# Performance work log

Measured on AMD Instinct MI355X. Metric: run time of the kernel, lower is better.

## Reference

```python
import jax, jax.numpy as jnp
import numpy as np

N, E, D = 100000, 600000, 128

def setup_inputs() -> dict:
    key = jax.random.key(0)
    ks = jax.random.split(key, 6)
    s = 1.0 / np.sqrt(D)
    return {
        "h": jax.random.normal(ks[0], (N, D), dtype=jnp.float32),
        "edge_index": jax.random.randint(ks[1], (2, E), 0, N, dtype=jnp.int64),
        "Wg": jax.random.normal(ks[2], (2 * D, D), dtype=jnp.float32) * s,
        "bg": jnp.zeros((D,), dtype=jnp.float32),
        "Ws": jax.random.normal(ks[3], (D, D), dtype=jnp.float32) * s,
        "bs": jnp.zeros((D,), dtype=jnp.float32),
        "Wr": jax.random.normal(ks[4], (D, D), dtype=jnp.float32) * s,
        "br": jnp.zeros((D,), dtype=jnp.float32),
    }

def reference(h, edge_index, Wg, bg, Ws, bs, Wr, br):
    send, rec = edge_index[0], edge_index[1]
    h_rec = h[rec]            # [E, D]
    h_send = h[send]          # [E, D]
    # gate: sigmoid(Linear(cat([h_rec, h_send])))  -- split W to avoid concat copy
    gate_in = h_rec @ Wg[:h.shape[1]] + h_send @ Wg[h.shape[1]:] + bg
    eta = jax.nn.sigmoid(gate_in)                      # [E, D]
    h_messages = eta * (h_send @ Ws + bs)              # [E, D]
    h_agg = jax.ops.segment_sum(h_messages, rec, num_segments=h.shape[0])
    return (h @ Wr + br) + h_agg
```

## Files before the change

### kernel.cpp

```cpp
#include <hip/hip_runtime.h>
#include <stdint.h>

#define FD 128

typedef __bf16 bf16x8 __attribute__((ext_vector_type(8)));
typedef unsigned short u16x8 __attribute__((ext_vector_type(8)));
typedef float  f32x16 __attribute__((ext_vector_type(16)));

__device__ __forceinline__ unsigned short f2bf(float f) {
    unsigned u = __float_as_uint(f);
    unsigned r = u + 0x7fffu + ((u >> 16) & 1u);
    return (unsigned short)(r >> 16);
}
__device__ __forceinline__ float bflo(unsigned u) { return __uint_as_float(u << 16); }
__device__ __forceinline__ float bfhi(unsigned u) { return __uint_as_float(u & 0xffff0000u); }


__global__ __launch_bounds__(256) void prep_kernel(
    const float* __restrict__ Wg,
    const float* __restrict__ Ws,
    const float* __restrict__ Wr,
    unsigned short* __restrict__ Wf)
{
    int wid = blockIdx.x * 256 + threadIdx.x;
    if (wid >= 512 * 128) return;
    int j  = wid & 7;
    int l  = (wid >> 3) & 63;
    int kt = (wid >> 9) & 7;
    int ct = wid >> 12;
    int k  = kt * 16 + (l >> 5) * 8 + j;
    int c  = ct * 32 + (l & 31);
    float v;
    if (c < 128)      v = Wg[k * FD + c];
    else if (c < 256) v = Wg[(128 + k) * FD + (c - 128)];
    else if (c < 384) v = Ws[k * FD + (c - 256)];
    else              v = Wr[k * FD + (c - 384)];
    Wf[wid] = f2bf(v);
}

__global__ __launch_bounds__(256, 4) void gemm_kernel(
    const float* __restrict__ h,
    const unsigned short* __restrict__ Wf,
    const float* __restrict__ bg,
    const float* __restrict__ bs,
    const float* __restrict__ br,
    unsigned short* __restrict__ A,
    unsigned short* __restrict__ BS,
    float* __restrict__ out,
    int N)
{
    __shared__ unsigned short Bsh[16384];

    const int w    = blockIdx.y;
    const int lane = threadIdx.x & 63;
    const int wid  = threadIdx.x >> 6;

    {
        const unsigned short* src = Wf + (size_t)w * 16384 + (size_t)threadIdx.x * 8;
        unsigned short* dst = Bsh + (size_t)threadIdx.x * 8;
        #pragma unroll
        for (int p = 0; p < 8; ++p) {
            __builtin_amdgcn_global_load_lds(
                (const __attribute__((address_space(1))) void*)(src + p * 2048),
                (__attribute__((address_space(3))) void*)(dst + p * 2048),
                16, 0, 0);
        }
    }

    const int col_l  = lane & 31;
    const int rhalf  = (lane >> 5) * 4;
    float bias[4];
    #pragma unroll
    for (int i = 0; i < 4; ++i) {
        int col = i * 32 + col_l;
        bias[i] = (w == 0) ? bg[col] : (w == 2) ? bs[col] : (w == 3) ? br[col] : 0.0f;
    }
    unsigned short* dst0 = (w == 0) ? A : (w == 2) ? (BS + 128) : BS;
    const size_t rstride = (w == 0) ? 128 : 256;

    __syncthreads();

    const int stride = gridDim.x * 128;
    for (int rb0 = blockIdx.x * 128; rb0 < N; rb0 += stride) {
        const int rb = rb0 + wid * 32;
        int arow = rb + (lane & 31);
        if (arow >= N) arow = N - 1;
        const float* aptr = h + (size_t)arow * FD + (lane >> 5) * 8;

        bf16x8 afrag[8];
        #pragma unroll
        for (int kt = 0; kt < 8; ++kt) {
            float4 f0 = *(const float4*)(aptr + kt * 16);
            float4 f1 = *(const float4*)(aptr + kt * 16 + 4);
            union { u16x8 u; bf16x8 b; } cv;
            cv.u[0] = f2bf(f0.x); cv.u[1] = f2bf(f0.y);
            cv.u[2] = f2bf(f0.z); cv.u[3] = f2bf(f0.w);
            cv.u[4] = f2bf(f1.x); cv.u[5] = f2bf(f1.y);
            cv.u[6] = f2bf(f1.z); cv.u[7] = f2bf(f1.w);
            afrag[kt] = cv.b;
        }

        f32x16 acc[4];
        #pragma unroll
        for (int i = 0; i < 4; ++i)
            #pragma unroll
            for (int r = 0; r < 16; ++r) acc[i][r] = 0.0f;

        #pragma unroll
        for (int kt = 0; kt < 8; ++kt) {
            #pragma unroll
            for (int i = 0; i < 4; ++i) {
                bf16x8 bfr = *(const bf16x8*)(Bsh + (size_t)((i * 8 + kt) * 64 + lane) * 8);
                acc[i] = __builtin_amdgcn_mfma_f32_32x32x16_bf16(
                             afrag[kt], bfr, acc[i], 0, 0, 0);
            }
        }

        const bool interior = (rb + 32 <= N);
        if (w == 3) {
            #pragma unroll
            for (int i = 0; i < 4; ++i) {
                int col = i * 32 + col_l;
                #pragma unroll
                for (int r = 0; r < 16; ++r) {
                    int row = rb + (r & 3) + 8 * (r >> 2) + rhalf;
                    if (interior || row < N)
                        out[(size_t)row * FD + col] = acc[i][r] + bias[i];
                }
            }
        } else {
            #pragma unroll
            for (int i = 0; i < 4; ++i) {
                int col = i * 32 + col_l;
                #pragma unroll
                for (int r = 0; r < 16; ++r) {
                    int row = rb + (r & 3) + 8 * (r >> 2) + rhalf;
                    if (interior || row < N)
                        dst0[(size_t)row * rstride + col] = f2bf(acc[i][r] + bias[i]);
                }
            }
        }
    }
}

__global__ __launch_bounds__(256) void hist_kernel(
    const int* __restrict__ idx, int* __restrict__ deg, int E)
{
    int e = blockIdx.x * 256 + threadIdx.x;
    if (e >= E) return;
    atomicAdd(&deg[idx[E + e]], 1);
}

__global__ __launch_bounds__(256) void scan1_kernel(
    const int* __restrict__ deg, int* __restrict__ partial, int N)
{
    __shared__ int sh[256];
    int base = blockIdx.x * 1024 + threadIdx.x * 4;
    int s = 0;
    #pragma unroll
    for (int j = 0; j < 4; ++j) s += (base + j < N) ? deg[base + j] : 0;
    sh[threadIdx.x] = s;
    __syncthreads();
    for (int ofs = 128; ofs > 0; ofs >>= 1) {
        if (threadIdx.x < ofs) sh[threadIdx.x] += sh[threadIdx.x + ofs];
        __syncthreads();
    }
    if (threadIdx.x == 0) partial[blockIdx.x] = sh[0];
}

__global__ __launch_bounds__(256) void scan2_kernel(int* __restrict__ partial, int nb)
{
    __shared__ int sh[256];
    int t = threadIdx.x;
    int p = (t < nb) ? partial[t] : 0;
    sh[t] = p;
    __syncthreads();
    for (int ofs = 1; ofs < 256; ofs <<= 1) {
        int x = (t >= ofs) ? sh[t - ofs] : 0;
        __syncthreads();
        sh[t] += x;
        __syncthreads();
    }
    if (t < nb) partial[t] = sh[t] - p;
}

__global__ __launch_bounds__(256) void scan3_kernel(
    int* __restrict__ deg, const int* __restrict__ partial, int N)
{
    __shared__ int sh[256];
    int base = blockIdx.x * 1024 + threadIdx.x * 4;
    int v[4];
    #pragma unroll
    for (int j = 0; j < 4; ++j) v[j] = (base + j < N) ? deg[base + j] : 0;
    int tsum = v[0] + v[1] + v[2] + v[3];
    sh[threadIdx.x] = tsum;
    __syncthreads();
    for (int ofs = 1; ofs < 256; ofs <<= 1) {
        int x = (threadIdx.x >= ofs) ? sh[threadIdx.x - ofs] : 0;
        __syncthreads();
        sh[threadIdx.x] += x;
        __syncthreads();
    }
    int run = partial[blockIdx.x] + sh[threadIdx.x] - tsum;
    #pragma unroll
    for (int j = 0; j < 4; ++j) {
        if (base + j < N) deg[base + j] = run;
        run += v[j];
    }
}

__global__ __launch_bounds__(256) void scatter_kernel(
    const int* __restrict__ idx, int* __restrict__ off,
    int* __restrict__ csr, int E)
{
    int e = blockIdx.x * 256 + threadIdx.x;
    if (e >= E) return;
    int s = idx[e];
    int r = idx[E + e];
    int pos = atomicAdd(&off[r], 1);
    csr[pos] = s;
}

__global__ __launch_bounds__(256) void aggregate_kernel(
    const int* __restrict__ off,
    const int* __restrict__ csr,
    const unsigned* __restrict__ A,
    const unsigned* __restrict__ BS,
    float* __restrict__ out,
    int N)
{
    int r = blockIdx.x * 4 + (threadIdx.x >> 6);
    if (r >= N) return;
    int lane = threadIdx.x & 63;

    int start = (r == 0) ? 0 : off[r - 1];
    int end   = off[r];
    if (start >= end) return;

    unsigned ua = A[(size_t)r * 64 + lane];
    float a0 = bflo(ua), a1 = bfhi(ua);
    float acc0 = 0.0f, acc1 = 0.0f;

    int i = start;
    for (; i + 3 < end; i += 4) {
        int s0 = csr[i], s1 = csr[i + 1], s2 = csr[i + 2], s3 = csr[i + 3];
        unsigned ub0 = BS[(size_t)s0 * 128 + lane];
        unsigned us0 = BS[(size_t)s0 * 128 + 64 + lane];
        unsigned ub1 = BS[(size_t)s1 * 128 + lane];
        unsigned us1 = BS[(size_t)s1 * 128 + 64 + lane];
        unsigned ub2 = BS[(size_t)s2 * 128 + lane];
        unsigned us2 = BS[(size_t)s2 * 128 + 64 + lane];
        unsigned ub3 = BS[(size_t)s3 * 128 + lane];
        unsigned us3 = BS[(size_t)s3 * 128 + 64 + lane];
        acc0 += bflo(us0) * __builtin_amdgcn_rcpf(1.0f + __expf(-(a0 + bflo(ub0))));
        acc1 += bfhi(us0) * __builtin_amdgcn_rcpf(1.0f + __expf(-(a1 + bfhi(ub0))));
        acc0 += bflo(us1) * __builtin_amdgcn_rcpf(1.0f + __expf(-(a0 + bflo(ub1))));
        acc1 += bfhi(us1) * __builtin_amdgcn_rcpf(1.0f + __expf(-(a1 + bfhi(ub1))));
        acc0 += bflo(us2) * __builtin_amdgcn_rcpf(1.0f + __expf(-(a0 + bflo(ub2))));
        acc1 += bfhi(us2) * __builtin_amdgcn_rcpf(1.0f + __expf(-(a1 + bfhi(ub2))));
        acc0 += bflo(us3) * __builtin_amdgcn_rcpf(1.0f + __expf(-(a0 + bflo(ub3))));
        acc1 += bfhi(us3) * __builtin_amdgcn_rcpf(1.0f + __expf(-(a1 + bfhi(ub3))));
    }
    for (; i < end; ++i) {
        int s0 = csr[i];
        unsigned ub0 = BS[(size_t)s0 * 128 + lane];
        unsigned us0 = BS[(size_t)s0 * 128 + 64 + lane];
        acc0 += bflo(us0) * __builtin_amdgcn_rcpf(1.0f + __expf(-(a0 + bflo(ub0))));
        acc1 += bfhi(us0) * __builtin_amdgcn_rcpf(1.0f + __expf(-(a1 + bfhi(ub0))));
    }

    float2* o = (float2*)(out + (size_t)r * FD + 2 * lane);
    float2 cur = *o;
    cur.x += acc0;
    cur.y += acc1;
    *o = cur;
}

extern "C" void kernel_launch(void* const* d_in, const int* in_sizes, int n_in,
                              void* d_out, int out_size, void* d_ws, size_t ws_size,
                              hipStream_t stream)
{
    const float* h  = (const float*)d_in[0];
    const int*   ei = (const int*)d_in[1];
    const float* Wg = (const float*)d_in[2];
    const float* bg = (const float*)d_in[3];
    const float* Ws = (const float*)d_in[4];
    const float* bs = (const float*)d_in[5];
    const float* Wr = (const float*)d_in[6];
    const float* br = (const float*)d_in[7];
    float* out = (float*)d_out;

    const int N = in_sizes[0] / FD;
    const int E = in_sizes[1] / 2;

    unsigned short* Wf  = (unsigned short*)d_ws;
    unsigned short* Abf = Wf + 512 * FD;
    unsigned short* BSb = Abf + (size_t)N * FD;
    int* deg     = (int*)(BSb + (size_t)N * 2 * FD);
    int* partial = deg + N;
    int* csr     = partial + 256;

    size_t need = (size_t)(512 * FD + 3ull * N * FD) * 2 + ((size_t)N + 256 + E) * 4;
    if (ws_size < need) return;

    const int nb = (N + 1023) / 1024;
    if (nb > 256) return;

    hipMemsetAsync(deg, 0, (size_t)N * 4, stream);

    prep_kernel<<<(512 * FD + 255) / 256, 256, 0, stream>>>(Wg, Ws, Wr, Wf);
    dim3 ggrid(256, 4);
    gemm_kernel<<<ggrid, 256, 0, stream>>>(h, Wf, bg, bs, br,
                                           Abf, BSb, out, N);
    hist_kernel<<<(E + 255) / 256, 256, 0, stream>>>(ei, deg, E);
    scan1_kernel<<<nb, 256, 0, stream>>>(deg, partial, N);
    scan2_kernel<<<1, 256, 0, stream>>>(partial, nb);
    scan3_kernel<<<nb, 256, 0, stream>>>(deg, partial, N);
    scatter_kernel<<<(E + 255) / 256, 256, 0, stream>>>(ei, deg, csr, E);
    aggregate_kernel<<<(N + 3) / 4, 256, 0, stream>>>(deg, csr,
                                                      (const unsigned*)Abf,
                                                      (const unsigned*)BSb,
                                                      out, N);
}
```

Measured before the change: 283.3 us.

## Fuse CSR build into one cooperative kernel with grid-wide syncs

Replaces the memset, histogram, three scan kernels and scatter with a single cooperative kernel of 1024 blocks that uses grid.sync between phases. This is meant to remove several kernel launch gaps and the separate memset. In exchange, each phase now runs grid-stride loops over fewer threads, and the grid barriers carry their own cost. The launch also depends on all 1024 blocks being co-resident.

```diff
diff --git a/kernel.cpp b/kernel.cpp
--- a/kernel.cpp
+++ b/kernel.cpp
@@ -1,5 +1,8 @@
 #include <hip/hip_runtime.h>
+#include <hip/hip_cooperative_groups.h>
 #include <stdint.h>
+
+namespace cg = cooperative_groups;
 
 #define FD 128
 
@@ -143,82 +146,85 @@
     }
 }
 
-__global__ __launch_bounds__(256) void hist_kernel(
-    const int* __restrict__ idx, int* __restrict__ deg, int E)
-{
-    int e = blockIdx.x * 256 + threadIdx.x;
-    if (e >= E) return;
-    atomicAdd(&deg[idx[E + e]], 1);
-}
-
-__global__ __launch_bounds__(256) void scan1_kernel(
-    const int* __restrict__ deg, int* __restrict__ partial, int N)
-{
+__global__ __launch_bounds__(256) void csr_kernel(
+    const int* __restrict__ idx,
+    int* __restrict__ deg,
+    int* __restrict__ partial,
+    int* __restrict__ csr,
+    int N, int E)
+{
+    cg::grid_group grid = cg::this_grid();
     __shared__ int sh[256];
-    int base = blockIdx.x * 1024 + threadIdx.x * 4;
-    int s = 0;
-    #pragma unroll
-    for (int j = 0; j < 4; ++j) s += (base + j < N) ? deg[base + j] : 0;
-    sh[threadIdx.x] = s;
-    __syncthreads();
-    for (int ofs = 128; ofs > 0; ofs >>= 1) {
-        if (threadIdx.x < ofs) sh[threadIdx.x] += sh[threadIdx.x + ofs];
+
+    const int tid  = blockIdx.x * 256 + threadIdx.x;
+    const int nthr = gridDim.x * 256;
+    const int nb   = (N + 1023) / 1024;
+
+    for (int i = tid; i < N; i += nthr) deg[i] = 0;
+    grid.sync();
+
+    for (int e = tid; e < E; e += nthr) atomicAdd(&deg[idx[E + e]], 1);
+    grid.sync();
+
+    if (blockIdx.x < nb) {
+        int base = blockIdx.x * 1024 + threadIdx.x * 4;
+        int s = 0;
+        #pragma unroll
+        for (int j = 0; j < 4; ++j) s += (base + j < N) ? deg[base + j] : 0;
+        sh[threadIdx.x] = s;
         __syncthreads();
-    }
-    if (threadIdx.x == 0) partial[blockIdx.x] = sh[0];
-}
-
-__global__ __launch_bounds__(256) void scan2_kernel(int* __restrict__ partial, int nb)
-{
-    __shared__ int sh[256];
-    int t = threadIdx.x;
-    int p = (t < nb) ? partial[t] : 0;
-    sh[t] = p;
-    __syncthreads();
-    for (int ofs = 1; ofs < 256; ofs <<= 1) {
-        int x = (t >= ofs) ? sh[t - ofs] : 0;
+        for (int ofs = 128; ofs > 0; ofs >>= 1) {
+            if (threadIdx.x < ofs) sh[threadIdx.x] += sh[threadIdx.x + ofs];
+            __syncthreads();
+        }
+        if (threadIdx.x == 0) partial[blockIdx.x] = sh[0];
+    }
+    grid.sync();
+
+    if (blockIdx.x == 0) {
+        int t = threadIdx.x;
+        int p = (t < nb) ? partial[t] : 0;
+        sh[t] = p;
         __syncthreads();
-        sh[t] += x;
+        for (int ofs = 1; ofs < 256; ofs <<= 1) {
+            int x = (t >= ofs) ? sh[t - ofs] : 0;
+            __syncthreads();
+            sh[t] += x;
+            __syncthreads();
+        }
+        if (t < nb) partial[t] = sh[t] - p;
+    }
+    grid.sync();
+
+    if (blockIdx.x < nb) {
+        int base = blockIdx.x * 1024 + threadIdx.x * 4;
+        int v[4];
+        #pragma unroll
+        for (int j = 0; j < 4; ++j) v[j] = (base + j < N) ? deg[base + j] : 0;
+        int tsum = v[0] + v[1] + v[2] + v[3];
+        sh[threadIdx.x] = tsum;
         __syncthreads();
-    }
-    if (t < nb) partial[t] = sh[t] - p;
-}
-
-__global__ __launch_bounds__(256) void scan3_kernel(
-    int* __restrict__ deg, const int* __restrict__ partial, int N)
-{
-    __shared__ int sh[256];
-    int base = blockIdx.x * 1024 + threadIdx.x * 4;
-    int v[4];
-    #pragma unroll
-    for (int j = 0; j < 4; ++j) v[j] = (base + j < N) ? deg[base + j] : 0;
-    int tsum = v[0] + v[1] + v[2] + v[3];
-    sh[threadIdx.x] = tsum;
-    __syncthreads();
-    for (int ofs = 1; ofs < 256; ofs <<= 1) {
-        int x = (threadIdx.x >= ofs) ? sh[threadIdx.x - ofs] : 0;
-        __syncthreads();
-        sh[threadIdx.x] += x;
-        __syncthreads();
-    }
-    int run = partial[blockIdx.x] + sh[threadIdx.x] - tsum;
-    #pragma unroll
-    for (int j = 0; j < 4; ++j) {
-        if (base + j < N) deg[base + j] = run;
-        run += v[j];
-    }
-}
-
-__global__ __launch_bounds__(256) void scatter_kernel(
-    const int* __restrict__ idx, int* __restrict__ off,
-    int* __restrict__ csr, int E)
-{
-    int e = blockIdx.x * 256 + threadIdx.x;
-    if (e >= E) return;
-    int s = idx[e];
-    int r = idx[E + e];
-    int pos = atomicAdd(&off[r], 1);
-    csr[pos] = s;
+        for (int ofs = 1; ofs < 256; ofs <<= 1) {
+            int x = (threadIdx.x >= ofs) ? sh[threadIdx.x - ofs] : 0;
+            __syncthreads();
+            sh[threadIdx.x] += x;
+            __syncthreads();
+        }
+        int run = partial[blockIdx.x] + sh[threadIdx.x] - tsum;
+        #pragma unroll
+        for (int j = 0; j < 4; ++j) {
+            if (base + j < N) deg[base + j] = run;
+            run += v[j];
+        }
+    }
+    grid.sync();
+
+    for (int e = tid; e < E; e += nthr) {
+        int s = idx[e];
+        int r = idx[E + e];
+        int pos = atomicAdd(&deg[r], 1);
+        csr[pos] = s;
+    }
 }
 
 __global__ __launch_bounds__(256) void aggregate_kernel(
@@ -306,17 +312,19 @@
     const int nb = (N + 1023) / 1024;
     if (nb > 256) return;
 
-    hipMemsetAsync(deg, 0, (size_t)N * 4, stream);
-
     prep_kernel<<<(512 * FD + 255) / 256, 256, 0, stream>>>(Wg, Ws, Wr, Wf);
     dim3 ggrid(256, 4);
     gemm_kernel<<<ggrid, 256, 0, stream>>>(h, Wf, bg, bs, br,
                                            Abf, BSb, out, N);
-    hist_kernel<<<(E + 255) / 256, 256, 0, stream>>>(ei, deg, E);
-    scan1_kernel<<<nb, 256, 0, stream>>>(deg, partial, N);
-    scan2_kernel<<<1, 256, 0, stream>>>(partial, nb);
-    scan3_kernel<<<nb, 256, 0, stream>>>(deg, partial, N);
-    scatter_kernel<<<(E + 255) / 256, 256, 0, stream>>>(ei, deg, csr, E);
+
+    {
+        int n = N, e = E;
+        void* args[] = { (void*)&ei, (void*)&deg, (void*)&partial,
+                         (void*)&csr, (void*)&n, (void*)&e };
+        hipLaunchCooperativeKernel((const void*)csr_kernel,
+                                   dim3(1024), dim3(256), args, 0, stream);
+    }
+
     aggregate_kernel<<<(N + 3) / 4, 256, 0, stream>>>(deg, csr,
                                                       (const unsigned*)Abf,
                                                       (const unsigned*)BSb,
```

New measurement: 766.9 us. 171% more time.

## Replace CSR build and segmented aggregation with per-edge atomic scatter

Applied to the files above, without the earlier changes.

Drops the histogram, three-pass scan and scatter kernels that built a receiver-sorted CSR. A single grid-stride kernel now handles one edge per wavefront, computes the gated message and atomically adds it into the output row. This removes five kernel launches and the memset. In exchange it issues 600k×128 float atomics to global memory instead of one coalesced read-modify-write per node, and the summation order becomes nondeterministic.

```diff
diff --git a/kernel.cpp b/kernel.cpp
--- a/kernel.cpp
+++ b/kernel.cpp
@@ -143,137 +143,31 @@
     }
 }
 
-__global__ __launch_bounds__(256) void hist_kernel(
-    const int* __restrict__ idx, int* __restrict__ deg, int E)
-{
-    int e = blockIdx.x * 256 + threadIdx.x;
-    if (e >= E) return;
-    atomicAdd(&deg[idx[E + e]], 1);
-}
-
-__global__ __launch_bounds__(256) void scan1_kernel(
-    const int* __restrict__ deg, int* __restrict__ partial, int N)
-{
-    __shared__ int sh[256];
-    int base = blockIdx.x * 1024 + threadIdx.x * 4;
-    int s = 0;
-    #pragma unroll
-    for (int j = 0; j < 4; ++j) s += (base + j < N) ? deg[base + j] : 0;
-    sh[threadIdx.x] = s;
-    __syncthreads();
-    for (int ofs = 128; ofs > 0; ofs >>= 1) {
-        if (threadIdx.x < ofs) sh[threadIdx.x] += sh[threadIdx.x + ofs];
-        __syncthreads();
-    }
-    if (threadIdx.x == 0) partial[blockIdx.x] = sh[0];
-}
-
-__global__ __launch_bounds__(256) void scan2_kernel(int* __restrict__ partial, int nb)
-{
-    __shared__ int sh[256];
-    int t = threadIdx.x;
-    int p = (t < nb) ? partial[t] : 0;
-    sh[t] = p;
-    __syncthreads();
-    for (int ofs = 1; ofs < 256; ofs <<= 1) {
-        int x = (t >= ofs) ? sh[t - ofs] : 0;
-        __syncthreads();
-        sh[t] += x;
-        __syncthreads();
-    }
-    if (t < nb) partial[t] = sh[t] - p;
-}
-
-__global__ __launch_bounds__(256) void scan3_kernel(
-    int* __restrict__ deg, const int* __restrict__ partial, int N)
-{
-    __shared__ int sh[256];
-    int base = blockIdx.x * 1024 + threadIdx.x * 4;
-    int v[4];
-    #pragma unroll
-    for (int j = 0; j < 4; ++j) v[j] = (base + j < N) ? deg[base + j] : 0;
-    int tsum = v[0] + v[1] + v[2] + v[3];
-    sh[threadIdx.x] = tsum;
-    __syncthreads();
-    for (int ofs = 1; ofs < 256; ofs <<= 1) {
-        int x = (threadIdx.x >= ofs) ? sh[threadIdx.x - ofs] : 0;
-        __syncthreads();
-        sh[threadIdx.x] += x;
-        __syncthreads();
-    }
-    int run = partial[blockIdx.x] + sh[threadIdx.x] - tsum;
-    #pragma unroll
-    for (int j = 0; j < 4; ++j) {
-        if (base + j < N) deg[base + j] = run;
-        run += v[j];
-    }
-}
-
-__global__ __launch_bounds__(256) void scatter_kernel(
-    const int* __restrict__ idx, int* __restrict__ off,
-    int* __restrict__ csr, int E)
-{
-    int e = blockIdx.x * 256 + threadIdx.x;
-    if (e >= E) return;
-    int s = idx[e];
-    int r = idx[E + e];
-    int pos = atomicAdd(&off[r], 1);
-    csr[pos] = s;
-}
-
-__global__ __launch_bounds__(256) void aggregate_kernel(
-    const int* __restrict__ off,
-    const int* __restrict__ csr,
+__global__ __launch_bounds__(256) void edge_agg_kernel(
+    const int* __restrict__ idx,
     const unsigned* __restrict__ A,
     const unsigned* __restrict__ BS,
     float* __restrict__ out,
-    int N)
-{
-    int r = blockIdx.x * 4 + (threadIdx.x >> 6);
-    if (r >= N) return;
-    int lane = threadIdx.x & 63;
-
-    int start = (r == 0) ? 0 : off[r - 1];
-    int end   = off[r];
-    if (start >= end) return;
-
-    unsigned ua = A[(size_t)r * 64 + lane];
-    float a0 = bflo(ua), a1 = bfhi(ua);
-    float acc0 = 0.0f, acc1 = 0.0f;
-
-    int i = start;
-    for (; i + 3 < end; i += 4) {
-        int s0 = csr[i], s1 = csr[i + 1], s2 = csr[i + 2], s3 = csr[i + 3];
-        unsigned ub0 = BS[(size_t)s0 * 128 + lane];
-        unsigned us0 = BS[(size_t)s0 * 128 + 64 + lane];
-        unsigned ub1 = BS[(size_t)s1 * 128 + lane];
-        unsigned us1 = BS[(size_t)s1 * 128 + 64 + lane];
-        unsigned ub2 = BS[(size_t)s2 * 128 + lane];
-        unsigned us2 = BS[(size_t)s2 * 128 + 64 + lane];
-        unsigned ub3 = BS[(size_t)s3 * 128 + lane];
-        unsigned us3 = BS[(size_t)s3 * 128 + 64 + lane];
-        acc0 += bflo(us0) * __builtin_amdgcn_rcpf(1.0f + __expf(-(a0 + bflo(ub0))));
-        acc1 += bfhi(us0) * __builtin_amdgcn_rcpf(1.0f + __expf(-(a1 + bfhi(ub0))));
-        acc0 += bflo(us1) * __builtin_amdgcn_rcpf(1.0f + __expf(-(a0 + bflo(ub1))));
-        acc1 += bfhi(us1) * __builtin_amdgcn_rcpf(1.0f + __expf(-(a1 + bfhi(ub1))));
-        acc0 += bflo(us2) * __builtin_amdgcn_rcpf(1.0f + __expf(-(a0 + bflo(ub2))));
-        acc1 += bfhi(us2) * __builtin_amdgcn_rcpf(1.0f + __expf(-(a1 + bfhi(ub2))));
-        acc0 += bflo(us3) * __builtin_amdgcn_rcpf(1.0f + __expf(-(a0 + bflo(ub3))));
-        acc1 += bfhi(us3) * __builtin_amdgcn_rcpf(1.0f + __expf(-(a1 + bfhi(ub3))));
-    }
-    for (; i < end; ++i) {
-        int s0 = csr[i];
-        unsigned ub0 = BS[(size_t)s0 * 128 + lane];
-        unsigned us0 = BS[(size_t)s0 * 128 + 64 + lane];
-        acc0 += bflo(us0) * __builtin_amdgcn_rcpf(1.0f + __expf(-(a0 + bflo(ub0))));
-        acc1 += bfhi(us0) * __builtin_amdgcn_rcpf(1.0f + __expf(-(a1 + bfhi(ub0))));
-    }
-
-    float2* o = (float2*)(out + (size_t)r * FD + 2 * lane);
-    float2 cur = *o;
-    cur.x += acc0;
-    cur.y += acc1;
-    *o = cur;
+    int E)
+{
+    const int lane = threadIdx.x & 63;
+    const int wv   = (blockIdx.x * 256 + threadIdx.x) >> 6;
+    const int nwv  = (gridDim.x * 256) >> 6;
+
+    for (int e = wv; e < E; e += nwv) {
+        int s = idx[e];
+        int r = idx[E + e];
+        unsigned ua = A[(size_t)r * 64 + lane];
+        unsigned ub = BS[(size_t)s * 128 + lane];
+        unsigned us = BS[(size_t)s * 128 + 64 + lane];
+        float g0 = bflo(ua) + bflo(ub);
+        float g1 = bfhi(ua) + bfhi(ub);
+        float m0 = bflo(us) * __builtin_amdgcn_rcpf(1.0f + __expf(-g0));
+        float m1 = bfhi(us) * __builtin_amdgcn_rcpf(1.0f + __expf(-g1));
+        float* o = out + (size_t)r * FD + 2 * lane;
+        atomicAdd(o,     m0);
+        atomicAdd(o + 1, m1);
+    }
 }
 
 extern "C" void kernel_launch(void* const* d_in, const int* in_sizes, int n_in,
@@ -296,29 +190,16 @@
     unsigned short* Wf  = (unsigned short*)d_ws;
     unsigned short* Abf = Wf + 512 * FD;
     unsigned short* BSb = Abf + (size_t)N * FD;
-    int* deg     = (int*)(BSb + (size_t)N * 2 * FD);
-    int* partial = deg + N;
-    int* csr     = partial + 256;
-
-    size_t need = (size_t)(512 * FD + 3ull * N * FD) * 2 + ((size_t)N + 256 + E) * 4;
+
+    size_t need = (size_t)(512 * FD + 3ull * N * FD) * 2;
     if (ws_size < need) return;
-
-    const int nb = (N + 1023) / 1024;
-    if (nb > 256) return;
-
-    hipMemsetAsync(deg, 0, (size_t)N * 4, stream);
 
     prep_kernel<<<(512 * FD + 255) / 256, 256, 0, stream>>>(Wg, Ws, Wr, Wf);
     dim3 ggrid(256, 4);
     gemm_kernel<<<ggrid, 256, 0, stream>>>(h, Wf, bg, bs, br,
                                            Abf, BSb, out, N);
-    hist_kernel<<<(E + 255) / 256, 256, 0, stream>>>(ei, deg, E);
-    scan1_kernel<<<nb, 256, 0, stream>>>(deg, partial, N);
-    scan2_kernel<<<1, 256, 0, stream>>>(partial, nb);
-    scan3_kernel<<<nb, 256, 0, stream>>>(deg, partial, N);
-    scatter_kernel<<<(E + 255) / 256, 256, 0, stream>>>(ei, deg, csr, E);
-    aggregate_kernel<<<(N + 3) / 4, 256, 0, stream>>>(deg, csr,
-                                                      (const unsigned*)Abf,
-                                                      (const unsigned*)BSb,
-                                                      out, N);
-}
+    edge_agg_kernel<<<2048, 256, 0, stream>>>(ei,
+                                              (const unsigned*)Abf,
+                                              (const unsigned*)BSb,
+                                              out, E);
+}
```

Result: slower. 653.2 us (+130.6%).

## Fuse degree zeroing, histogram and scan stages to cut kernel launches

Applied to the files above, without the earlier changes.

Moves zeroing of the degree and partial arrays into the weight-prep kernel, which replaces the separate memset. The degree histogram now runs as an extra blockIdx.y slice of the GEMM launch, so it overlaps with the matmul blocks. The three-kernel scan becomes one single-pass scan in which each block publishes its aggregate with a flag bit and later blocks spin-wait on those flags. This removes several launches and serialization gaps. The cost is a dependency on earlier scan blocks being resident or finished, and atomic traffic competing with the GEMM.

```diff
diff --git a/kernel.cpp b/kernel.cpp
--- a/kernel.cpp
+++ b/kernel.cpp
@@ -20,9 +20,14 @@
     const float* __restrict__ Wg,
     const float* __restrict__ Ws,
     const float* __restrict__ Wr,
-    unsigned short* __restrict__ Wf)
+    unsigned short* __restrict__ Wf,
+    int* __restrict__ deg,
+    int* __restrict__ partial,
+    int N)
 {
     int wid = blockIdx.x * 256 + threadIdx.x;
+    for (int i = wid; i < N; i += 65536) deg[i] = 0;
+    if (wid < 256) partial[wid] = 0;
     if (wid >= 512 * 128) return;
     int j  = wid & 7;
     int l  = (wid >> 3) & 63;
@@ -47,9 +52,17 @@
     unsigned short* __restrict__ A,
     unsigned short* __restrict__ BS,
     float* __restrict__ out,
-    int N)
+    const int* __restrict__ idx,
+    int* __restrict__ deg,
+    int N, int E)
 {
     __shared__ unsigned short Bsh[16384];
+
+    if (blockIdx.y == 4) {
+        int t = blockIdx.x * 256 + threadIdx.x;
+        for (int e = t; e < E; e += 65536) atomicAdd(&deg[idx[E + e]], 1);
+        return;
+    }
 
     const int w    = blockIdx.y;
     const int lane = threadIdx.x & 63;
@@ -143,65 +156,40 @@
     }
 }
 
-__global__ __launch_bounds__(256) void hist_kernel(
-    const int* __restrict__ idx, int* __restrict__ deg, int E)
-{
-    int e = blockIdx.x * 256 + threadIdx.x;
-    if (e >= E) return;
-    atomicAdd(&deg[idx[E + e]], 1);
-}
-
-__global__ __launch_bounds__(256) void scan1_kernel(
-    const int* __restrict__ deg, int* __restrict__ partial, int N)
+__global__ __launch_bounds__(256) void scan_kernel(
+    int* __restrict__ deg, unsigned* __restrict__ partial, int N)
 {
     __shared__ int sh[256];
-    int base = blockIdx.x * 1024 + threadIdx.x * 4;
-    int s = 0;
-    #pragma unroll
-    for (int j = 0; j < 4; ++j) s += (base + j < N) ? deg[base + j] : 0;
-    sh[threadIdx.x] = s;
-    __syncthreads();
-    for (int ofs = 128; ofs > 0; ofs >>= 1) {
-        if (threadIdx.x < ofs) sh[threadIdx.x] += sh[threadIdx.x + ofs];
-        __syncthreads();
-    }
-    if (threadIdx.x == 0) partial[blockIdx.x] = sh[0];
-}
-
-__global__ __launch_bounds__(256) void scan2_kernel(int* __restrict__ partial, int nb)
-{
-    __shared__ int sh[256];
-    int t = threadIdx.x;
-    int p = (t < nb) ? partial[t] : 0;
-    sh[t] = p;
-    __syncthreads();
-    for (int ofs = 1; ofs < 256; ofs <<= 1) {
-        int x = (t >= ofs) ? sh[t - ofs] : 0;
-        __syncthreads();
-        sh[t] += x;
-        __syncthreads();
-    }
-    if (t < nb) partial[t] = sh[t] - p;
-}
-
-__global__ __launch_bounds__(256) void scan3_kernel(
-    int* __restrict__ deg, const int* __restrict__ partial, int N)
-{
-    __shared__ int sh[256];
-    int base = blockIdx.x * 1024 + threadIdx.x * 4;
+    __shared__ int sh2[256];
+    const int bid = blockIdx.x;
+    const int tid = threadIdx.x;
+    int base = bid * 1024 + tid * 4;
     int v[4];
     #pragma unroll
     for (int j = 0; j < 4; ++j) v[j] = (base + j < N) ? deg[base + j] : 0;
     int tsum = v[0] + v[1] + v[2] + v[3];
-    sh[threadIdx.x] = tsum;
+    sh[tid] = tsum;
     __syncthreads();
     for (int ofs = 1; ofs < 256; ofs <<= 1) {
-        int x = (threadIdx.x >= ofs) ? sh[threadIdx.x - ofs] : 0;
+        int x = (tid >= ofs) ? sh[tid - ofs] : 0;
         __syncthreads();
-        sh[threadIdx.x] += x;
+        sh[tid] += x;
         __syncthreads();
     }
-    int run = partial[blockIdx.x] + sh[threadIdx.x] - tsum;
+    if (tid == 0) atomicExch(&partial[bid], 0x80000000u | (unsigned)sh[255]);
+    int myagg = 0;
+    if (tid < bid) {
+        unsigned p;
+        do { p = atomicAdd(&partial[tid], 0u); } while (!(p & 0x80000000u));
+        myagg = (int)(p & 0x7fffffffu);
+    }
+    sh2[tid] = myagg;
+    __syncthreads();
+    for (int ofs = 128; ofs > 0; ofs >>= 1) {
+        if (tid < ofs) sh2[tid] += sh2[tid + ofs];
+        __syncthreads();
+    }
+    int run = sh2[0] + sh[tid] - tsum;
     #pragma unroll
     for (int j = 0; j < 4; ++j) {
         if (base + j < N) deg[base + j] = run;
@@ -306,16 +294,11 @@
     const int nb = (N + 1023) / 1024;
     if (nb > 256) return;
 
-    hipMemsetAsync(deg, 0, (size_t)N * 4, stream);
-
-    prep_kernel<<<(512 * FD + 255) / 256, 256, 0, stream>>>(Wg, Ws, Wr, Wf);
-    dim3 ggrid(256, 4);
+    prep_kernel<<<256, 256, 0, stream>>>(Wg, Ws, Wr, Wf, deg, partial, N);
+    dim3 ggrid(256, 5);
     gemm_kernel<<<ggrid, 256, 0, stream>>>(h, Wf, bg, bs, br,
-                                           Abf, BSb, out, N);
-    hist_kernel<<<(E + 255) / 256, 256, 0, stream>>>(ei, deg, E);
-    scan1_kernel<<<nb, 256, 0, stream>>>(deg, partial, N);
-    scan2_kernel<<<1, 256, 0, stream>>>(partial, nb);
-    scan3_kernel<<<nb, 256, 0, stream>>>(deg, partial, N);
+                                           Abf, BSb, out, ei, deg, N, E);
+    scan_kernel<<<nb, 256, 0, stream>>>(deg, (unsigned*)partial, N);
     scatter_kernel<<<(E + 255) / 256, 256, 0, stream>>>(ei, deg, csr, E);
     aggregate_kernel<<<(N + 3) / 4, 256, 0, stream>>>(deg, csr,
                                                       (const unsigned*)Abf,
```

New measurement: 270.7 us. -4.4%, faster.
